# Kernel tuning notes

Measured on AMD Instinct MI355X. Metric: run time of the kernel, lower is better.

Reference implementation:

```python
import jax, jax.numpy as jnp
import numpy as np

B, N, K, D = 4, 32768, 16, 8  # batch, points, neighbors, output channels
EPS = 1e-6  # BatchNorm eps from module


def setup_inputs() -> dict:
    key = jax.random.key(0)
    ks = jax.random.split(key, 6)
    coords = jax.random.normal(ks[0], (B, N, 3), jnp.float32)
    features = jax.random.normal(ks[1], (B, D, N, 1), jnp.float32)
    knn_idx = jax.random.randint(ks[2], (B, N, K), 0, N, dtype=jnp.int64)
    knn_dist = jax.random.uniform(ks[3], (B, N, K), jnp.float32)
    mask = jnp.ones((B, N), jnp.int32)  # all-valid points
    conv_w = jax.random.normal(ks[4], (D, 10), jnp.float32) * 0.1  # 1x1 Conv2d weight (out,in)
    conv_b = jnp.zeros((D,), jnp.float32)
    bn_gamma = jnp.ones((D,), jnp.float32)
    bn_beta = jnp.zeros((D,), jnp.float32)
    return {
        "coords": coords, "features": features, "knn_idx": knn_idx,
        "knn_dist": knn_dist, "mask": mask, "conv_w": conv_w,
        "conv_b": conv_b, "bn_gamma": bn_gamma, "bn_beta": bn_beta,
    }


def reference(coords, features, knn_idx, knn_dist, mask, conv_w, conv_b, bn_gamma, bn_beta):
    # coords: (B,N,3); knn_idx/knn_dist: (B,N,K); features: (B,D,N,1); mask: (B,N)
    idx = jnp.clip(knn_idx, 0, None)
    # gather neighbor coords per batch: (B,N,K,3)
    neighbors = jax.vmap(lambda c, i: c[i])(coords, idx)
    center = jnp.broadcast_to(coords[:, :, None, :], neighbors.shape)  # (B,N,K,3)
    # masked_fill invalid points' distances with +inf (mask==0)
    dist = jnp.where(mask[:, :, None] == 0, jnp.inf, knn_dist)
    # channel-last concat: [center(3), neighbors(3), diff(3), dist(1)] -> (B,N,K,10)
    feat = jnp.concatenate(
        [center, neighbors, center - neighbors, dist[..., None]], axis=-1)
    # 1x1 conv == per-position linear 10 -> D, output layout (B,D,N,K)
    x = jnp.einsum('bnkc,dc->bdnk', feat, conv_w) + conv_b[None, :, None, None]
    # BatchNorm2d in training mode: biased batch stats over (B,N,K) per channel
    mean = x.mean(axis=(0, 2, 3), keepdims=True)
    var = x.var(axis=(0, 2, 3), keepdims=True)
    x = (x - mean) * jax.lax.rsqrt(var + EPS)
    x = x * bn_gamma[None, :, None, None] + bn_beta[None, :, None, None]
    x = jax.nn.relu(x)
    # expand features (B,D,N,1) -> (B,D,N,K) and concat on channel dim
    f = jnp.broadcast_to(features, (x.shape[0], features.shape[1], x.shape[2], x.shape[3]))
    return jnp.concatenate([x, f], axis=1)  # (B, 2D, N, K)
```

## Files before the change

### kernel.cpp

```cpp
#include <hip/hip_runtime.h>

#define NB 4
#define NP 32768
#define NK 16
#define ND 8
#define EPSV 1e-6f


__global__ __launch_bounds__(256) void lse_stats(
    const float* __restrict__ coords,
    const int*   __restrict__ knn_idx,
    const float* __restrict__ knn_dist,
    const int*   __restrict__ mask,
    const float* __restrict__ conv_w,
    const float* __restrict__ conv_b,
    float*       __restrict__ accum)
{
    const int gid = blockIdx.x * 256 + threadIdx.x;
    const int b = gid >> 15;
    const int n = gid & (NP - 1);

    float a0[ND], a1[ND], a2[ND], e0[ND], e1[ND], e2[ND], w9[ND], cb[ND];
#pragma unroll
    for (int d = 0; d < ND; ++d) {
        const float* w = conv_w + d * 10;
        float w0 = w[0], w1 = w[1], w2 = w[2];
        float w3 = w[3], w4 = w[4], w5 = w[5];
        float w6 = w[6], w7 = w[7], w8 = w[8];
        a0[d] = w0 + w6; a1[d] = w1 + w7; a2[d] = w2 + w8;
        e0[d] = w3 - w6; e1[d] = w4 - w7; e2[d] = w5 - w8;
        w9[d] = w[9];    cb[d] = conv_b[d];
    }

    const float* cbase = coords + (size_t)b * NP * 3;
    const float cx = cbase[n * 3 + 0];
    const float cy = cbase[n * 3 + 1];
    const float cz = cbase[n * 3 + 2];
    const int   mk = mask[b * NP + n];

    const int4*   idx4 = (const int4*)(knn_idx + ((size_t)gid) * NK);
    const float4* dst4 = (const float4*)(knn_dist + ((size_t)gid) * NK);

    float cterm[ND];
#pragma unroll
    for (int d = 0; d < ND; ++d)
        cterm[d] = fmaf(a0[d], cx, fmaf(a1[d], cy, fmaf(a2[d], cz, cb[d])));

    float sum[ND], sq[ND];
#pragma unroll
    for (int d = 0; d < ND; ++d) { sum[d] = 0.f; sq[d] = 0.f; }

#pragma unroll
    for (int q = 0; q < 4; ++q) {
        int4   id = idx4[q];
        float4 dv = dst4[q];
        int   js[4] = {id.x, id.y, id.z, id.w};
        float dsv[4] = {dv.x, dv.y, dv.z, dv.w};
#pragma unroll
        for (int t = 0; t < 4; ++t) {
            int j = js[t] < 0 ? 0 : js[t];
            const float* nb = cbase + (size_t)j * 3;
            float nx = nb[0], ny = nb[1], nz = nb[2];
            float dist = (mk == 0) ? __builtin_inff() : dsv[t];
#pragma unroll
            for (int d = 0; d < ND; ++d) {
                float x = fmaf(e0[d], nx, fmaf(e1[d], ny,
                          fmaf(e2[d], nz, fmaf(w9[d], dist, cterm[d]))));
                sum[d] += x;
                sq[d]  = fmaf(x, x, sq[d]);
            }
        }
    }

#pragma unroll
    for (int d = 0; d < ND; ++d) {
        float s = sum[d], s2 = sq[d];
#pragma unroll
        for (int off = 32; off > 0; off >>= 1) {
            s  += __shfl_down(s,  off);
            s2 += __shfl_down(s2, off);
        }
        sum[d] = s; sq[d] = s2;
    }

    __shared__ float lds[4][16];
    const int wave = threadIdx.x >> 6;
    const int lane = threadIdx.x & 63;
    if (lane == 0) {
#pragma unroll
        for (int d = 0; d < ND; ++d) {
            lds[wave][d]     = sum[d];
            lds[wave][8 + d] = sq[d];
        }
    }
    __syncthreads();
    if (threadIdx.x < 16) {
        float v = lds[0][threadIdx.x] + lds[1][threadIdx.x]
                + lds[2][threadIdx.x] + lds[3][threadIdx.x];
        atomicAdd(&accum[threadIdx.x], v);
    }
}

__global__ __launch_bounds__(256) void lse_main(
    const float* __restrict__ coords,
    const float* __restrict__ features,
    const int*   __restrict__ knn_idx,
    const float* __restrict__ knn_dist,
    const int*   __restrict__ mask,
    const float* __restrict__ conv_w,
    const float* __restrict__ conv_b,
    const float* __restrict__ bn_gamma,
    const float* __restrict__ bn_beta,
    const float* __restrict__ accum,
    float*       __restrict__ out)
{
    const int gid = blockIdx.x * 256 + threadIdx.x;
    const int b     = gid >> 19;
    const int local = gid & (NP * NK - 1);
    const int n     = local >> 4;

    const float invM = 1.0f / (float)(NB * NP * NK);
    float scale[ND], shift[ND];
#pragma unroll
    for (int d = 0; d < ND; ++d) {
        float mean = accum[d] * invM;
        float var  = fmaf(-mean, mean, accum[8 + d] * invM);
        float g    = bn_gamma[d] * rsqrtf(var + EPSV);
        scale[d] = g;
        shift[d] = fmaf(-mean, g, bn_beta[d]);
    }

    float a0[ND], a1[ND], a2[ND], e0[ND], e1[ND], e2[ND], w9[ND], cb[ND];
#pragma unroll
    for (int d = 0; d < ND; ++d) {
        const float* w = conv_w + d * 10;
        float w0 = w[0], w1 = w[1], w2 = w[2];
        float w3 = w[3], w4 = w[4], w5 = w[5];
        float w6 = w[6], w7 = w[7], w8 = w[8];
        a0[d] = w0 + w6; a1[d] = w1 + w7; a2[d] = w2 + w8;
        e0[d] = w3 - w6; e1[d] = w4 - w7; e2[d] = w5 - w8;
        w9[d] = w[9];    cb[d] = conv_b[d];
    }

    const float* cbase = coords + (size_t)b * NP * 3;
    const float cx = cbase[n * 3 + 0];
    const float cy = cbase[n * 3 + 1];
    const float cz = cbase[n * 3 + 2];

    int j = knn_idx[gid]; j = j < 0 ? 0 : j;
    const float nx = cbase[j * 3 + 0];
    const float ny = cbase[j * 3 + 1];
    const float nz = cbase[j * 3 + 2];

    const int   mk   = mask[b * NP + n];
    const float dist = (mk == 0) ? __builtin_inff() : knn_dist[gid];

    const size_t obase = (size_t)b * (2 * ND) * NP * NK + (size_t)local;
    const size_t cstr  = (size_t)NP * NK;

#pragma unroll
    for (int d = 0; d < ND; ++d) {
        float x = fmaf(a0[d], cx, fmaf(a1[d], cy, fmaf(a2[d], cz,
                  fmaf(e0[d], nx, fmaf(e1[d], ny, fmaf(e2[d], nz,
                  fmaf(w9[d], dist, cb[d])))))));
        float y = fmaf(x, scale[d], shift[d]);
        out[obase + (size_t)d * cstr] = fmaxf(y, 0.f);
    }

    const float* fbase = features + (size_t)b * ND * NP;
#pragma unroll
    for (int d = 0; d < ND; ++d) {
        out[obase + (size_t)(ND + d) * cstr] = fbase[d * NP + n];
    }
}

extern "C" void kernel_launch(void* const* d_in, const int* in_sizes, int n_in,
                              void* d_out, int out_size, void* d_ws, size_t ws_size,
                              hipStream_t stream) {
    const float* coords   = (const float*)d_in[0];
    const float* features = (const float*)d_in[1];
    const int*   knn_idx  = (const int*)  d_in[2];
    const float* knn_dist = (const float*)d_in[3];
    const int*   mask     = (const int*)  d_in[4];
    const float* conv_w   = (const float*)d_in[5];
    const float* conv_b   = (const float*)d_in[6];
    const float* bn_gamma = (const float*)d_in[7];
    const float* bn_beta  = (const float*)d_in[8];
    float* out   = (float*)d_out;
    float* accum = (float*)d_ws;

    hipMemsetAsync(accum, 0, 16 * sizeof(float), stream);

    lse_stats<<<(NB * NP) / 256, 256, 0, stream>>>(
        coords, knn_idx, knn_dist, mask, conv_w, conv_b, accum);

    lse_main<<<(NB * NP * NK) / 256, 256, 0, stream>>>(
        coords, features, knn_idx, knn_dist, mask, conv_w, conv_b,
        bn_gamma, bn_beta, accum, out);
}
```

Baseline: 202.8 us.

## Stage pre-BN conv outputs in fp16 and apply BatchNorm in a streaming pass

The first pass now computes the conv outputs once, accumulates the BN statistics, writes the broadcast feature half of the output, and stages the pre-normalization values in an fp16 workspace buffer (or in the output itself if the workspace is too small). The second pass becomes a pure streaming scale/shift/ReLU over the staged values. This removes the second gather of knn indices and neighbor coordinates and the recomputation of the conv. In exchange it adds a write and re-read of the staged tensor, and fp16 staging rounds the pre-BN values.

```diff
diff --git a/kernel.cpp b/kernel.cpp
--- a/kernel.cpp
+++ b/kernel.cpp
@@ -1,4 +1,5 @@
 #include <hip/hip_runtime.h>
+#include <hip/hip_fp16.h>
 
 #define NB 4
 #define NP 32768
@@ -7,18 +8,23 @@
 #define EPSV 1e-6f
 
 
-__global__ __launch_bounds__(256) void lse_stats(
+__global__ __launch_bounds__(256) void lse_pass1(
     const float* __restrict__ coords,
+    const float* __restrict__ features,
     const int*   __restrict__ knn_idx,
     const float* __restrict__ knn_dist,
     const int*   __restrict__ mask,
     const float* __restrict__ conv_w,
     const float* __restrict__ conv_b,
-    float*       __restrict__ accum)
+    float*       __restrict__ accum,
+    __half*      __restrict__ xstage,
+    float*       __restrict__ out)
 {
     const int gid = blockIdx.x * 256 + threadIdx.x;
-    const int b = gid >> 15;
-    const int n = gid & (NP - 1);
+    const int b   = gid >> 17;
+    const int r   = gid & (NP * 4 - 1);
+    const int n   = r >> 2;
+    const int k0  = (r & 3) * 4;
 
     float a0[ND], a1[ND], a2[ND], e0[ND], e1[ND], e2[ND], w9[ND], cb[ND];
 #pragma unroll
@@ -33,43 +39,63 @@
     }
 
     const float* cbase = coords + (size_t)b * NP * 3;
-    const float cx = cbase[n * 3 + 0];
-    const float cy = cbase[n * 3 + 1];
-    const float cz = cbase[n * 3 + 2];
-    const int   mk = mask[b * NP + n];
-
-    const int4*   idx4 = (const int4*)(knn_idx + ((size_t)gid) * NK);
-    const float4* dst4 = (const float4*)(knn_dist + ((size_t)gid) * NK);
-
-    float cterm[ND];
-#pragma unroll
-    for (int d = 0; d < ND; ++d)
-        cterm[d] = fmaf(a0[d], cx, fmaf(a1[d], cy, fmaf(a2[d], cz, cb[d])));
-
+    const float  cx = cbase[n * 3 + 0];
+    const float  cy = cbase[n * 3 + 1];
+    const float  cz = cbase[n * 3 + 2];
+
+    const size_t p  = ((size_t)(b * NP + n)) * NK + k0;
+    const int4   id = *(const int4*)(knn_idx + p);
+    float4       dv = *(const float4*)(knn_dist + p);
+    if (mask[b * NP + n] == 0) {
+        dv.x = dv.y = dv.z = dv.w = __builtin_inff();
+    }
+
+    const int   js[4] = {id.x < 0 ? 0 : id.x, id.y < 0 ? 0 : id.y,
+                         id.z < 0 ? 0 : id.z, id.w < 0 ? 0 : id.w};
+    const float ds[4] = {dv.x, dv.y, dv.z, dv.w};
+
+    float xv[4][ND];
     float sum[ND], sq[ND];
 #pragma unroll
     for (int d = 0; d < ND; ++d) { sum[d] = 0.f; sq[d] = 0.f; }
 
 #pragma unroll
-    for (int q = 0; q < 4; ++q) {
-        int4   id = idx4[q];
-        float4 dv = dst4[q];
-        int   js[4] = {id.x, id.y, id.z, id.w};
-        float dsv[4] = {dv.x, dv.y, dv.z, dv.w};
-#pragma unroll
-        for (int t = 0; t < 4; ++t) {
-            int j = js[t] < 0 ? 0 : js[t];
-            const float* nb = cbase + (size_t)j * 3;
-            float nx = nb[0], ny = nb[1], nz = nb[2];
-            float dist = (mk == 0) ? __builtin_inff() : dsv[t];
-#pragma unroll
-            for (int d = 0; d < ND; ++d) {
-                float x = fmaf(e0[d], nx, fmaf(e1[d], ny,
-                          fmaf(e2[d], nz, fmaf(w9[d], dist, cterm[d]))));
-                sum[d] += x;
-                sq[d]  = fmaf(x, x, sq[d]);
-            }
-        }
+    for (int t = 0; t < 4; ++t) {
+        const float* nb = cbase + (size_t)js[t] * 3;
+        const float  nx = nb[0], ny = nb[1], nz = nb[2];
+#pragma unroll
+        for (int d = 0; d < ND; ++d) {
+            float x = fmaf(a0[d], cx, fmaf(a1[d], cy, fmaf(a2[d], cz,
+                      fmaf(e0[d], nx, fmaf(e1[d], ny, fmaf(e2[d], nz,
+                      fmaf(w9[d], ds[t], cb[d])))))));
+            xv[t][d] = x;
+            sum[d] += x;
+            sq[d]   = fmaf(x, x, sq[d]);
+        }
+    }
+
+    if (xstage) {
+#pragma unroll
+        for (int d = 0; d < ND; ++d) {
+            __half2* o2 = (__half2*)(xstage +
+                ((((size_t)(b * ND + d)) * NP + n) << 4) + k0);
+            o2[0] = __floats2half2_rn(xv[0][d], xv[1][d]);
+            o2[1] = __floats2half2_rn(xv[2][d], xv[3][d]);
+        }
+    } else {
+#pragma unroll
+        for (int d = 0; d < ND; ++d) {
+            *(float4*)(out + ((((size_t)(b * 2 * ND + d)) * NP + n) << 4) + k0) =
+                make_float4(xv[0][d], xv[1][d], xv[2][d], xv[3][d]);
+        }
+    }
+
+    const float* fb = features + (size_t)b * ND * NP;
+#pragma unroll
+    for (int d = 0; d < ND; ++d) {
+        const float v = fb[d * NP + n];
+        *(float4*)(out + ((((size_t)(b * 2 * ND + ND + d)) * NP + n) << 4) + k0) =
+            make_float4(v, v, v, v);
     }
 
 #pragma unroll
@@ -82,10 +108,8 @@
         }
         sum[d] = s; sq[d] = s2;
     }
-
     __shared__ float lds[4][16];
-    const int wave = threadIdx.x >> 6;
-    const int lane = threadIdx.x & 63;
+    const int wave = threadIdx.x >> 6, lane = threadIdx.x & 63;
     if (lane == 0) {
 #pragma unroll
         for (int d = 0; d < ND; ++d) {
@@ -101,77 +125,54 @@
     }
 }
 
-__global__ __launch_bounds__(256) void lse_main(
-    const float* __restrict__ coords,
-    const float* __restrict__ features,
-    const int*   __restrict__ knn_idx,
-    const float* __restrict__ knn_dist,
-    const int*   __restrict__ mask,
-    const float* __restrict__ conv_w,
-    const float* __restrict__ conv_b,
-    const float* __restrict__ bn_gamma,
-    const float* __restrict__ bn_beta,
-    const float* __restrict__ accum,
-    float*       __restrict__ out)
+__global__ __launch_bounds__(256) void lse_pass2(
+    const float*  __restrict__ accum,
+    const float*  __restrict__ bn_gamma,
+    const float*  __restrict__ bn_beta,
+    const __half* __restrict__ xstage,
+    float*        __restrict__ out)
 {
-    const int gid = blockIdx.x * 256 + threadIdx.x;
-    const int b     = gid >> 19;
-    const int local = gid & (NP * NK - 1);
-    const int n     = local >> 4;
+    const int    gid = blockIdx.x * 256 + threadIdx.x;
+    const size_t s0  = (size_t)gid * 8;
+    const int    d   = (int)((s0 >> 19) & 7);
+    const int    b   = (int)(s0 >> 22);
+    const size_t inp = s0 & ((1u << 19) - 1);
+    const size_t o   = (((size_t)(b * 2 * ND + d)) << 19) | inp;
 
     const float invM = 1.0f / (float)(NB * NP * NK);
-    float scale[ND], shift[ND];
-#pragma unroll
-    for (int d = 0; d < ND; ++d) {
-        float mean = accum[d] * invM;
-        float var  = fmaf(-mean, mean, accum[8 + d] * invM);
-        float g    = bn_gamma[d] * rsqrtf(var + EPSV);
-        scale[d] = g;
-        shift[d] = fmaf(-mean, g, bn_beta[d]);
-    }
-
-    float a0[ND], a1[ND], a2[ND], e0[ND], e1[ND], e2[ND], w9[ND], cb[ND];
-#pragma unroll
-    for (int d = 0; d < ND; ++d) {
-        const float* w = conv_w + d * 10;
-        float w0 = w[0], w1 = w[1], w2 = w[2];
-        float w3 = w[3], w4 = w[4], w5 = w[5];
-        float w6 = w[6], w7 = w[7], w8 = w[8];
-        a0[d] = w0 + w6; a1[d] = w1 + w7; a2[d] = w2 + w8;
-        e0[d] = w3 - w6; e1[d] = w4 - w7; e2[d] = w5 - w8;
-        w9[d] = w[9];    cb[d] = conv_b[d];
-    }
-
-    const float* cbase = coords + (size_t)b * NP * 3;
-    const float cx = cbase[n * 3 + 0];
-    const float cy = cbase[n * 3 + 1];
-    const float cz = cbase[n * 3 + 2];
-
-    int j = knn_idx[gid]; j = j < 0 ? 0 : j;
-    const float nx = cbase[j * 3 + 0];
-    const float ny = cbase[j * 3 + 1];
-    const float nz = cbase[j * 3 + 2];
-
-    const int   mk   = mask[b * NP + n];
-    const float dist = (mk == 0) ? __builtin_inff() : knn_dist[gid];
-
-    const size_t obase = (size_t)b * (2 * ND) * NP * NK + (size_t)local;
-    const size_t cstr  = (size_t)NP * NK;
-
-#pragma unroll
-    for (int d = 0; d < ND; ++d) {
-        float x = fmaf(a0[d], cx, fmaf(a1[d], cy, fmaf(a2[d], cz,
-                  fmaf(e0[d], nx, fmaf(e1[d], ny, fmaf(e2[d], nz,
-                  fmaf(w9[d], dist, cb[d])))))));
-        float y = fmaf(x, scale[d], shift[d]);
-        out[obase + (size_t)d * cstr] = fmaxf(y, 0.f);
-    }
-
-    const float* fbase = features + (size_t)b * ND * NP;
-#pragma unroll
-    for (int d = 0; d < ND; ++d) {
-        out[obase + (size_t)(ND + d) * cstr] = fbase[d * NP + n];
-    }
+    const float mean = accum[d] * invM;
+    const float var  = fmaf(-mean, mean, accum[8 + d] * invM);
+    const float g    = bn_gamma[d] * rsqrtf(var + EPSV);
+    const float sh   = fmaf(-mean, g, bn_beta[d]);
+
+    float x[8];
+    if (xstage) {
+        const float4 raw = *(const float4*)(xstage + s0);
+        const __half2* h = (const __half2*)&raw;
+#pragma unroll
+        for (int q = 0; q < 4; ++q) {
+            float2 f = __half22float2(h[q]);
+            x[2 * q]     = f.x;
+            x[2 * q + 1] = f.y;
+        }
+    } else {
+        const float4 v0 = *(const float4*)(out + o);
+        const float4 v1 = *(const float4*)(out + o + 4);
+        x[0] = v0.x; x[1] = v0.y; x[2] = v0.z; x[3] = v0.w;
+        x[4] = v1.x; x[5] = v1.y; x[6] = v1.z; x[7] = v1.w;
+    }
+
+    float4 r0, r1;
+    r0.x = fmaxf(fmaf(x[0], g, sh), 0.f);
+    r0.y = fmaxf(fmaf(x[1], g, sh), 0.f);
+    r0.z = fmaxf(fmaf(x[2], g, sh), 0.f);
+    r0.w = fmaxf(fmaf(x[3], g, sh), 0.f);
+    r1.x = fmaxf(fmaf(x[4], g, sh), 0.f);
+    r1.y = fmaxf(fmaf(x[5], g, sh), 0.f);
+    r1.z = fmaxf(fmaf(x[6], g, sh), 0.f);
+    r1.w = fmaxf(fmaf(x[7], g, sh), 0.f);
+    *(float4*)(out + o)     = r0;
+    *(float4*)(out + o + 4) = r1;
 }
 
 extern "C" void kernel_launch(void* const* d_in, const int* in_sizes, int n_in,
@@ -189,12 +190,16 @@
     float* out   = (float*)d_out;
     float* accum = (float*)d_ws;
 
-    hipMemsetAsync(accum, 0, 16 * sizeof(float), stream);
-
-    lse_stats<<<(NB * NP) / 256, 256, 0, stream>>>(
-        coords, knn_idx, knn_dist, mask, conv_w, conv_b, accum);
-
-    lse_main<<<(NB * NP * NK) / 256, 256, 0, stream>>>(
+    hipMemsetAsync(d_ws, 0, 64, stream);
+
+    __half* xstage = nullptr;
+    const size_t need = 256 + (size_t)NB * ND * NP * NK * sizeof(__half);
+    if (ws_size >= need) xstage = (__half*)((char*)d_ws + 256);
+
+    lse_pass1<<<(NB * NP * 4) / 256, 256, 0, stream>>>(
         coords, features, knn_idx, knn_dist, mask, conv_w, conv_b,
-        bn_gamma, bn_beta, accum, out);
+        accum, xstage, out);
+
+    lse_pass2<<<(NB * ND * NP * NK / 8) / 256, 256, 0, stream>>>(
+        accum, bn_gamma, bn_beta, xstage, out);
 }
```

Measured after the change: 196.3 us. 1.03x faster.
